# Optimization experiments

Measured on AMD Instinct MI355X. Metric: run time of the kernel, lower is better.

Reference implementation:

```python
import jax, jax.numpy as jnp
import numpy as np

ASPECT = 1.0
SCALE = 0.3
MIN_PATCH_H = 60.0
EPS = 1e-6


def _make_patch_boxes(boxes, H, W):
    # Patcher.create: per detected box, compute [ymin_patch, xmin_patch, patch_h, patch_w]
    ymin, xmin, ymax, xmax = jnp.split(boxes, 4, axis=-1)
    h = ymax - ymin
    w = xmax - xmin
    pw = h * SCALE
    ph = ASPECT * pw
    oy = ymin + h / 2.0
    ox = xmin + w / 2.0
    yp = jnp.maximum(oy - ph / 2.0, 0.0)
    xp = jnp.maximum(ox - pw / 2.0, 0.0)
    yp = jnp.where(yp + ph > H, H - ph, yp)
    xp = jnp.where(xp + pw > W, W - pw, xp)
    return jnp.concatenate([yp, xp, ph, pw], axis=-1)  # [B, N, 4]


def _bilinear(src, rel_y, rel_x, out_h, out_w):
    # tf.image.resize bilinear (half-pixel centers): sample src [P,P,3] at the
    # grid of an (out_h, out_w) resize, evaluated at all H/W image offsets.
    P = src.shape[0]
    sy = jnp.clip((rel_y + 0.5) * P / out_h - 0.5, 0.0, P - 1.0)  # [H]
    sx = jnp.clip((rel_x + 0.5) * P / out_w - 0.5, 0.0, P - 1.0)  # [W]
    y0 = jnp.floor(sy).astype(jnp.int32); y1 = jnp.minimum(y0 + 1, P - 1)
    x0 = jnp.floor(sx).astype(jnp.int32); x1 = jnp.minimum(x0 + 1, P - 1)
    wy = (sy - y0.astype(sy.dtype))[:, None, None]
    wx = (sx - x0.astype(sx.dtype))[None, :, None]
    top = (1.0 - wx) * src[y0[:, None], x0[None, :]] + wx * src[y0[:, None], x1[None, :]]
    bot = (1.0 - wx) * src[y1[:, None], x0[None, :]] + wx * src[y1[:, None], x1[None, :]]
    return (1.0 - wy) * top + wy * bot  # [H, W, 3]


def _forward(images, boxes, patch):
    B, H, W, _ = images.shape
    pboxes = _make_patch_boxes(boxes, float(H), float(W))  # [B, N, 4]
    valid = pboxes[..., 2] > MIN_PATCH_H                    # gather_nd filter
    p_mean = patch.mean((0, 1))
    p_std = patch.std((0, 1)) + EPS
    ys = jnp.arange(H, dtype=jnp.int32)
    xs = jnp.arange(W, dtype=jnp.int32)

    def per_image(image, pbs, vls):
        # serial while_loop over patches: later patches overwrite earlier ones,
        # and histogram match uses the current (already-patched) background.
        def step(img, bv):
            pb, v = bv
            pbi = pb.astype(jnp.int32)  # tf.cast truncation
            y0, x0, ph, pw = pbi[0], pbi[1], pbi[2], pbi[3]
            in_y = (ys >= y0) & (ys < y0 + ph)
            in_x = (xs >= x0) & (xs < x0 + pw)
            mask = in_y[:, None] & in_x[None, :]            # [H, W]
            mf = mask[..., None].astype(img.dtype)
            cnt = jnp.maximum(mask.sum().astype(img.dtype), 1.0)
            bg_mean = (img * mf).sum((0, 1)) / cnt
            bg_std = jnp.sqrt((((img - bg_mean) ** 2) * mf).sum((0, 1)) / cnt) + EPS
            # histogram match (per-channel moment matching) of patch to background
            matched = (patch - p_mean) / p_std * bg_std + bg_mean
            phf = jnp.maximum(ph.astype(img.dtype), 1.0)
            pwf = jnp.maximum(pw.astype(img.dtype), 1.0)
            sampled = _bilinear(matched,
                                (ys - y0).astype(img.dtype),
                                (xs - x0).astype(img.dtype), phf, pwf)
            img = jnp.where(mask[..., None] & v, sampled, img)
            return img, None

        img, _ = jax.lax.scan(step, image, (pbs, vls))
        return img

    return jax.vmap(per_image)(images, pboxes, valid)


def setup_inputs() -> dict:
    key = jax.random.key(0)
    k1, k2, k3 = jax.random.split(key, 3)
    B, N, H, W, P = 16, 16, 512, 512, 512
    images = jax.random.normal(k1, (B, H, W, 3), dtype=jnp.float32)
    u = jax.random.uniform(k2, (B, N, 4), dtype=jnp.float32)
    ymin = u[..., 0] * (H - 320)
    xmin = u[..., 1] * (W - 320)
    h = 150.0 + u[..., 2] * 150.0
    w = 150.0 + u[..., 3] * 150.0
    boxes = jnp.stack([ymin, xmin, ymin + h, xmin + w], axis=-1)
    patch = jax.random.normal(k3, (P, P, 3), dtype=jnp.float32) * 0.5
    return {"images": images, "boxes": boxes, "patch": patch}


def reference(images, boxes, patch):
    return _forward(images, boxes, patch)
```

## Files before the change

kernel.cpp:

```cpp
#include <hip/hip_runtime.h>
#include <math.h>

#define IMG_H 512
#define IMG_W 512
#define PSIZE 512
#define NIMG 16
#define NBOX 16
#define RED_BLOCKS 256
#define ZSPLIT 4

#define WS_PMEAN 0
#define WS_PSTD  3
#define WS_PART  6
#define WS_PAIR  (6 + RED_BLOCKS * 6)
#define WS_COEF  (WS_PAIR + NIMG * NBOX * 17 * ZSPLIT * 8)

struct BoxGeo { int y0, x0, ph, pw, valid; };

__device__ __forceinline__ BoxGeo make_geo(const float* bx) {
    float ymin = bx[0], xmin = bx[1], ymax = bx[2], xmax = bx[3];
    float h = ymax - ymin, w = xmax - xmin;
    float pwf = h * 0.3f;
    float phf = 1.0f * pwf;
    float oy = ymin + h * 0.5f;
    float ox = xmin + w * 0.5f;
    float yp = fmaxf(oy - phf * 0.5f, 0.0f);
    float xp = fmaxf(ox - pwf * 0.5f, 0.0f);
    if (yp + phf > (float)IMG_H) yp = (float)IMG_H - phf;
    if (xp + pwf > (float)IMG_W) xp = (float)IMG_W - pwf;
    BoxGeo g;
    g.y0 = (int)yp; g.x0 = (int)xp;
    g.ph = (int)phf; g.pw = (int)pwf;
    g.valid = (phf > 60.0f) ? 1 : 0;
    return g;
}

__device__ __forceinline__ void bsample(const float* __restrict__ patch,
                                        int relY, int relX, float phf, float pwf,
                                        float s[3]) {
    float sy = ((float)relY + 0.5f) * (float)PSIZE / phf - 0.5f;
    sy = fminf(fmaxf(sy, 0.0f), (float)(PSIZE - 1));
    float sx = ((float)relX + 0.5f) * (float)PSIZE / pwf - 0.5f;
    sx = fminf(fmaxf(sx, 0.0f), (float)(PSIZE - 1));
    int y0 = (int)floorf(sy);
    int y1 = min(y0 + 1, PSIZE - 1);
    int x0 = (int)floorf(sx);
    int x1 = min(x0 + 1, PSIZE - 1);
    float wy = sy - (float)y0;
    float wx = sx - (float)x0;
    const float* p00 = patch + (y0 * PSIZE + x0) * 3;
    const float* p01 = patch + (y0 * PSIZE + x1) * 3;
    const float* p10 = patch + (y1 * PSIZE + x0) * 3;
    const float* p11 = patch + (y1 * PSIZE + x1) * 3;
#pragma unroll
    for (int c = 0; c < 3; ++c) {
        float top = (1.f - wx) * p00[c] + wx * p01[c];
        float bot = (1.f - wx) * p10[c] + wx * p11[c];
        s[c] = (1.f - wy) * top + wy * bot;
    }
}

template<int N, int NWAVES>
__device__ __forceinline__ void block_reduceN(float v[N]) {
    __shared__ float lds[NWAVES][N];
    const int lane = threadIdx.x & 63;
    const int wave = threadIdx.x >> 6;
    __syncthreads();
#pragma unroll
    for (int k = 0; k < N; ++k) {
#pragma unroll
        for (int off = 32; off > 0; off >>= 1)
            v[k] += __shfl_down(v[k], off, 64);
    }
    if (lane == 0) {
#pragma unroll
        for (int k = 0; k < N; ++k) lds[wave][k] = v[k];
    }
    __syncthreads();
    if (wave == 0) {
#pragma unroll
        for (int k = 0; k < N; ++k) {
            float x = (lane < NWAVES) ? lds[lane][k] : 0.0f;
#pragma unroll
            for (int off = 32; off > 0; off >>= 1)
                x += __shfl_down(x, off, 64);
            if (lane == 0) lds[0][k] = x;
        }
    }
    __syncthreads();
#pragma unroll
    for (int k = 0; k < N; ++k) v[k] = lds[0][k];
}

__global__ void patch_stats_partial(const float* __restrict__ patch,
                                    float* __restrict__ ws) {
    const int g = blockIdx.x * 256 + threadIdx.x;
    const float4* p4 = (const float4*)patch;
    float4 a = p4[3 * g], b = p4[3 * g + 1], c = p4[3 * g + 2];
    float v[6];
    v[0] = a.x + a.w + b.z + c.y;
    v[1] = a.y + b.x + b.w + c.z;
    v[2] = a.z + b.y + c.x + c.w;
    v[3] = a.x*a.x + a.w*a.w + b.z*b.z + c.y*c.y;
    v[4] = a.y*a.y + b.x*b.x + b.w*b.w + c.z*c.z;
    v[5] = a.z*a.z + b.y*b.y + c.x*c.x + c.w*c.w;
    block_reduceN<6, 4>(v);
    if (threadIdx.x == 0) {
        float* o = ws + WS_PART + blockIdx.x * 6;
#pragma unroll
        for (int k = 0; k < 6; ++k) o[k] = v[k];
    }
}

__global__ void patch_stats_final(float* __restrict__ ws) {
    float v[6];
    const float* p = ws + WS_PART + threadIdx.x * 6;
#pragma unroll
    for (int k = 0; k < 6; ++k) v[k] = p[k];
    block_reduceN<6, 4>(v);
    if (threadIdx.x == 0) {
        const float n = (float)(PSIZE * PSIZE);
#pragma unroll
        for (int c = 0; c < 3; ++c) {
            float m = v[c] / n;
            float var = v[3 + c] / n - m * m;
            ws[WS_PMEAN + c] = m;
            ws[WS_PSTD + c] = sqrtf(fmaxf(var, 0.f)) + 1e-6f;
        }
    }
}

__launch_bounds__(256)
__global__ void pair_sums(const float* __restrict__ images,
                          const float* __restrict__ boxes,
                          const float* __restrict__ patch,
                          float* __restrict__ ws) {
    const int bi = blockIdx.x;
    const int j_idx = blockIdx.y;
    const int z = blockIdx.z;
    const int b = bi >> 4, i = bi & 15;
    if (j_idx > i) return;

    __shared__ BoxGeo geo[NBOX];
    if (threadIdx.x < NBOX)
        geo[threadIdx.x] = make_geo(boxes + (b * NBOX + threadIdx.x) * 4);
    __syncthreads();

    const BoxGeo gi = geo[i];
    if (!gi.valid) return;

    float* o = ws + WS_PAIR + (((size_t)(b * NBOX + i) * 17 + j_idx) * ZSPLIT + z) * 8;
    const int j = j_idx - 1;

    int ry0 = gi.y0, rx0 = gi.x0;
    int ry1 = gi.y0 + gi.ph, rx1 = gi.x0 + gi.pw;
    int jy0 = 0, jx0 = 0; float jphf = 1.f, jpwf = 1.f;
    if (j >= 0) {
        const BoxGeo gj = geo[j];
        if (!gj.valid) {
            if (threadIdx.x == 0) { for (int k = 0; k < 7; ++k) o[k] = 0.f; }
            return;
        }
        ry0 = max(ry0, gj.y0); rx0 = max(rx0, gj.x0);
        ry1 = min(ry1, gj.y0 + gj.ph); rx1 = min(rx1, gj.x0 + gj.pw);
        jy0 = gj.y0; jx0 = gj.x0;
        jphf = (float)gj.ph; jpwf = (float)gj.pw;
    }
    const int rw = rx1 - rx0, rh = ry1 - ry0;
    if (rw <= 0 || rh <= 0) {
        if (threadIdx.x == 0) { for (int k = 0; k < 7; ++k) o[k] = 0.f; }
        return;
    }
    const int n = rw * rh;
    const float* img = images + (size_t)b * IMG_H * IMG_W * 3;

    float v[7] = {0.f, 0.f, 0.f, 0.f, 0.f, 0.f, 0.f};
    for (int t = z * 256 + threadIdx.x; t < n; t += 256 * ZSPLIT) {
        const int y = ry0 + t / rw;
        const int x = rx0 + t % rw;
        bool inc = true;
        for (int k = j + 1; k < i; ++k) {
            const BoxGeo gk = geo[k];
            if (gk.valid && y >= gk.y0 && y < gk.y0 + gk.ph &&
                x >= gk.x0 && x < gk.x0 + gk.pw) { inc = false; break; }
        }
        if (inc) {
            float s[3];
            if (j >= 0) {
                bsample(patch, y - jy0, x - jx0, jphf, jpwf, s);
            } else {
                const float* p = img + ((size_t)y * IMG_W + x) * 3;
                s[0] = p[0]; s[1] = p[1]; s[2] = p[2];
            }
            v[0] += 1.f;
            v[1] += s[0]; v[2] += s[1]; v[3] += s[2];
            v[4] += s[0]*s[0]; v[5] += s[1]*s[1]; v[6] += s[2]*s[2];
        }
    }
    block_reduceN<7, 4>(v);
    if (threadIdx.x == 0) {
#pragma unroll
        for (int k = 0; k < 7; ++k) o[k] = v[k];
    }
}

__global__ void solve_coeffs(const float* __restrict__ boxes,
                             float* __restrict__ ws) {
    const int b = blockIdx.x;
    const int lane = threadIdx.x;

    BoxGeo g = make_geo(boxes + (b * NBOX + (lane < NBOX ? lane : NBOX - 1)) * 4);
    float pm[3], ps[3];
#pragma unroll
    for (int c = 0; c < 3; ++c) { pm[c] = ws[WS_PMEAN + c]; ps[c] = ws[WS_PSTD + c]; }

    float sc[3] = {0.f, 0.f, 0.f}, of[3] = {0.f, 0.f, 0.f};

    for (int i = 0; i < NBOX; ++i) {
        const int valid_i = __shfl(g.valid, i, 64);
        if (!valid_i) continue;

        float cnt = 0.f, s1[3] = {0.f,0.f,0.f}, s2[3] = {0.f,0.f,0.f};
        if (lane <= i) {
            const float* p = ws + WS_PAIR +
                ((size_t)(b * NBOX + i) * 17 + lane) * ZSPLIT * 8;
#pragma unroll
            for (int zz = 0; zz < ZSPLIT; ++zz) {
                cnt   += p[zz*8 + 0];
                s1[0] += p[zz*8 + 1]; s1[1] += p[zz*8 + 2]; s1[2] += p[zz*8 + 3];
                s2[0] += p[zz*8 + 4]; s2[1] += p[zz*8 + 5]; s2[2] += p[zz*8 + 6];
            }
        }
        float ts[3], tq[3];
#pragma unroll
        for (int c = 0; c < 3; ++c) {
            if (lane == 0) { ts[c] = s1[c]; tq[c] = s2[c]; }
            else {
                ts[c] = sc[c] * s1[c] + of[c] * cnt;
                tq[c] = sc[c]*sc[c]*s2[c] + 2.f*sc[c]*of[c]*s1[c] + of[c]*of[c]*cnt;
            }
        }
#pragma unroll
        for (int c = 0; c < 3; ++c) {
#pragma unroll
            for (int off = 16; off > 0; off >>= 1) {
                ts[c] += __shfl_down(ts[c], off, 32);
                tq[c] += __shfl_down(tq[c], off, 32);
            }
        }
        const int phi = __shfl(g.ph, i, 64);
        const int pwi = __shfl(g.pw, i, 64);
        const float cntf = fmaxf((float)(phi * pwi), 1.0f);
        float nsc[3] = {0.f,0.f,0.f}, nof[3] = {0.f,0.f,0.f};
        if (lane == 0) {
#pragma unroll
            for (int c = 0; c < 3; ++c) {
                float mean = ts[c] / cntf;
                float var = tq[c] / cntf - mean * mean;
                float sd = sqrtf(fmaxf(var, 0.f)) + 1e-6f;
                nsc[c] = sd / ps[c];
                nof[c] = mean - pm[c] * nsc[c];
            }
        }
#pragma unroll
        for (int c = 0; c < 3; ++c) {
            float bs = __shfl(nsc[c], 0, 64);
            float bo = __shfl(nof[c], 0, 64);
            if (lane == i + 1) { sc[c] = bs; of[c] = bo; }
            if (lane == 0) {
                ws[WS_COEF + (size_t)(b * NBOX + i) * 8 + c] = bs;
                ws[WS_COEF + (size_t)(b * NBOX + i) * 8 + 3 + c] = bo;
            }
        }
    }
}

__launch_bounds__(256)
__global__ void render(const float* __restrict__ images,
                       const float* __restrict__ boxes,
                       const float* __restrict__ patch,
                       const float* __restrict__ ws,
                       float* __restrict__ out) {
    const int b = blockIdx.y;
    __shared__ BoxGeo geo[NBOX];
    __shared__ float coef[NBOX][6];
    if (threadIdx.x < NBOX)
        geo[threadIdx.x] = make_geo(boxes + (b * NBOX + threadIdx.x) * 4);
    if (threadIdx.x < NBOX * 6) {
        int i = threadIdx.x / 6, c = threadIdx.x % 6;
        coef[i][c] = ws[WS_COEF + (size_t)(b * NBOX + i) * 8 + c];
    }
    __syncthreads();

    const int q = blockIdx.x * 256 + threadIdx.x;
    const int p0 = q << 2;
    const int y = p0 >> 9, x0 = p0 & 511;

    const float4* src = (const float4*)(images + (size_t)b * IMG_H * IMG_W * 3);
    float4* dst = (float4*)(out + (size_t)b * IMG_H * IMG_W * 3);

    float4 f[3];
    f[0] = src[3*q]; f[1] = src[3*q + 1]; f[2] = src[3*q + 2];
    float* r = (float*)f;

#pragma unroll
    for (int u = 0; u < 4; ++u) {
        const int x = x0 + u;
        int last = -1;
        for (int j = NBOX - 1; j >= 0; --j) {
            const BoxGeo g = geo[j];
            if (g.valid && y >= g.y0 && y < g.y0 + g.ph &&
                x >= g.x0 && x < g.x0 + g.pw) { last = j; break; }
        }
        if (last >= 0) {
            const BoxGeo g = geo[last];
            float s[3];
            bsample(patch, y - g.y0, x - g.x0, (float)g.ph, (float)g.pw, s);
            r[3*u + 0] = s[0] * coef[last][0] + coef[last][3];
            r[3*u + 1] = s[1] * coef[last][1] + coef[last][4];
            r[3*u + 2] = s[2] * coef[last][2] + coef[last][5];
        }
    }
    dst[3*q] = f[0]; dst[3*q + 1] = f[1]; dst[3*q + 2] = f[2];
}

extern "C" void kernel_launch(void* const* d_in, const int* in_sizes, int n_in,
                              void* d_out, int out_size, void* d_ws, size_t ws_size,
                              hipStream_t stream) {
    const float* images = (const float*)d_in[0];
    const float* boxes  = (const float*)d_in[1];
    const float* patch  = (const float*)d_in[2];
    float* out = (float*)d_out;
    float* ws  = (float*)d_ws;

    patch_stats_partial<<<RED_BLOCKS, 256, 0, stream>>>(patch, ws);
    patch_stats_final<<<1, RED_BLOCKS, 0, stream>>>(ws);
    pair_sums<<<dim3(NIMG * NBOX, 17, ZSPLIT), 256, 0, stream>>>(images, boxes, patch, ws);
    solve_coeffs<<<NIMG, 64, 0, stream>>>(boxes, ws);
    render<<<dim3(IMG_H * IMG_W / 4 / 256, NIMG), 256, 0, stream>>>(images, boxes, patch, ws, out);
}
```

Before: 106.0 us.

## Replace full-image render with memcpy plus per-box decal scatter; precompute geometry tasks

```diff
diff --git a/kernel.cpp b/kernel.cpp
--- a/kernel.cpp
+++ b/kernel.cpp
@@ -7,13 +7,17 @@
 #define NIMG 16
 #define NBOX 16
 #define RED_BLOCKS 256
-#define ZSPLIT 4
+#define Z0 8
+#define ZJ 4
+#define SLOTS 72
 
 #define WS_PMEAN 0
 #define WS_PSTD  3
 #define WS_PART  6
-#define WS_PAIR  (6 + RED_BLOCKS * 6)
-#define WS_COEF  (WS_PAIR + NIMG * NBOX * 17 * ZSPLIT * 8)
+#define WS_GEO   1544
+#define WS_TASK  2568
+#define WS_PAIR  37384
+#define WS_COEF  (WS_PAIR + 256 * SLOTS * 8)
 
 struct BoxGeo { int y0, x0, ph, pw, valid; };
 
@@ -92,6 +96,46 @@
     for (int k = 0; k < N; ++k) v[k] = lds[0][k];
 }
 
+__global__ void setup_geo(const float* __restrict__ boxes,
+                          float* __restrict__ ws) {
+    int* iws = (int*)ws;
+    const int tid = threadIdx.x;
+    if (tid < NIMG * NBOX) {
+        BoxGeo g = make_geo(boxes + tid * 4);
+        ((int4*)(iws + WS_GEO))[tid] =
+            make_int4(g.y0, g.x0, g.valid ? g.ph : -1, g.pw);
+    }
+    for (int t = tid; t < NIMG * NBOX * 17; t += 256) {
+        const int bi = t / 17, j_idx = t % 17;
+        const int b = bi >> 4, i = bi & 15;
+        int d[8] = {0, 0, 0, 0, 0, 0, -1, 0};
+        if (j_idx <= i) {
+            BoxGeo gi = make_geo(boxes + (b * NBOX + i) * 4);
+            if (gi.valid) {
+                int ry0 = gi.y0, rx0 = gi.x0;
+                int ry1 = gi.y0 + gi.ph, rx1 = gi.x0 + gi.pw;
+                bool ok = true;
+                if (j_idx >= 1) {
+                    BoxGeo gj = make_geo(boxes + (b * NBOX + j_idx - 1) * 4);
+                    if (!gj.valid) ok = false;
+                    else {
+                        ry0 = max(ry0, gj.y0); rx0 = max(rx0, gj.x0);
+                        ry1 = min(ry1, gj.y0 + gj.ph);
+                        rx1 = min(rx1, gj.x0 + gj.pw);
+                        d[4] = gj.y0; d[5] = gj.x0; d[6] = gj.ph; d[7] = gj.pw;
+                    }
+                }
+                if (ok && ry1 > ry0 && rx1 > rx0) {
+                    d[0] = ry0; d[1] = rx0; d[2] = rx1 - rx0; d[3] = ry1 - ry0;
+                }
+            }
+        }
+        int* o = iws + WS_TASK + t * 8;
+#pragma unroll
+        for (int k = 0; k < 8; ++k) o[k] = d[k];
+    }
+}
+
 __global__ void patch_stats_partial(const float* __restrict__ patch,
                                     float* __restrict__ ws) {
     const int g = blockIdx.x * 256 + threadIdx.x;
@@ -132,61 +176,43 @@
 
 __launch_bounds__(256)
 __global__ void pair_sums(const float* __restrict__ images,
-                          const float* __restrict__ boxes,
                           const float* __restrict__ patch,
                           float* __restrict__ ws) {
-    const int bi = blockIdx.x;
-    const int j_idx = blockIdx.y;
-    const int z = blockIdx.z;
-    const int b = bi >> 4, i = bi & 15;
+    const int bi = blockIdx.x, j_idx = blockIdx.y, z = blockIdx.z;
+    const int i = bi & 15;
     if (j_idx > i) return;
-
-    __shared__ BoxGeo geo[NBOX];
+    if (j_idx >= 1 && z >= ZJ) return;
+    const int* iws = (const int*)ws;
+    const int* d = iws + WS_TASK + (bi * 17 + j_idx) * 8;
+    const int rw = d[2];
+    if (rw <= 0) return;
+    const int ry0 = d[0], rx0 = d[1], rh = d[3];
+    const int jy0 = d[4], jx0 = d[5], jph = d[6], jpw = d[7];
+
+    __shared__ int4 sgeo[NBOX];
     if (threadIdx.x < NBOX)
-        geo[threadIdx.x] = make_geo(boxes + (b * NBOX + threadIdx.x) * 4);
-    __syncthreads();
-
-    const BoxGeo gi = geo[i];
-    if (!gi.valid) return;
-
-    float* o = ws + WS_PAIR + (((size_t)(b * NBOX + i) * 17 + j_idx) * ZSPLIT + z) * 8;
-    const int j = j_idx - 1;
-
-    int ry0 = gi.y0, rx0 = gi.x0;
-    int ry1 = gi.y0 + gi.ph, rx1 = gi.x0 + gi.pw;
-    int jy0 = 0, jx0 = 0; float jphf = 1.f, jpwf = 1.f;
-    if (j >= 0) {
-        const BoxGeo gj = geo[j];
-        if (!gj.valid) {
-            if (threadIdx.x == 0) { for (int k = 0; k < 7; ++k) o[k] = 0.f; }
-            return;
-        }
-        ry0 = max(ry0, gj.y0); rx0 = max(rx0, gj.x0);
-        ry1 = min(ry1, gj.y0 + gj.ph); rx1 = min(rx1, gj.x0 + gj.pw);
-        jy0 = gj.y0; jx0 = gj.x0;
-        jphf = (float)gj.ph; jpwf = (float)gj.pw;
-    }
-    const int rw = rx1 - rx0, rh = ry1 - ry0;
-    if (rw <= 0 || rh <= 0) {
-        if (threadIdx.x == 0) { for (int k = 0; k < 7; ++k) o[k] = 0.f; }
-        return;
-    }
+        sgeo[threadIdx.x] =
+            ((const int4*)(iws + WS_GEO))[(bi >> 4) * NBOX + threadIdx.x];
+    __syncthreads();
+
     const int n = rw * rh;
-    const float* img = images + (size_t)b * IMG_H * IMG_W * 3;
+    const float* img = images + (size_t)(bi >> 4) * IMG_H * IMG_W * 3;
+    const float jphf = (float)jph, jpwf = (float)jpw;
+    const int nz = (j_idx == 0) ? Z0 : ZJ;
 
     float v[7] = {0.f, 0.f, 0.f, 0.f, 0.f, 0.f, 0.f};
-    for (int t = z * 256 + threadIdx.x; t < n; t += 256 * ZSPLIT) {
+    for (int t = z * 256 + threadIdx.x; t < n; t += 256 * nz) {
         const int y = ry0 + t / rw;
         const int x = rx0 + t % rw;
         bool inc = true;
-        for (int k = j + 1; k < i; ++k) {
-            const BoxGeo gk = geo[k];
-            if (gk.valid && y >= gk.y0 && y < gk.y0 + gk.ph &&
-                x >= gk.x0 && x < gk.x0 + gk.pw) { inc = false; break; }
+        for (int k = j_idx; k < i; ++k) {
+            const int4 g = sgeo[k];
+            if (g.z > 0 && y >= g.x && y < g.x + g.z &&
+                x >= g.y && x < g.y + g.w) { inc = false; break; }
         }
         if (inc) {
             float s[3];
-            if (j >= 0) {
+            if (jph > 0) {
                 bsample(patch, y - jy0, x - jx0, jphf, jpwf, s);
             } else {
                 const float* p = img + ((size_t)y * IMG_W + x) * 3;
@@ -199,6 +225,8 @@
     }
     block_reduceN<7, 4>(v);
     if (threadIdx.x == 0) {
+        const int slot = (j_idx == 0) ? z : (Z0 + (j_idx - 1) * ZJ + z);
+        float* o = ws + WS_PAIR + ((size_t)bi * SLOTS + slot) * 8;
 #pragma unroll
         for (int k = 0; k < 7; ++k) o[k] = v[k];
     }
@@ -222,10 +250,11 @@
 
         float cnt = 0.f, s1[3] = {0.f,0.f,0.f}, s2[3] = {0.f,0.f,0.f};
         if (lane <= i) {
+            const int slot0 = (lane == 0) ? 0 : (Z0 + (lane - 1) * ZJ);
+            const int nz = (lane == 0) ? Z0 : ZJ;
             const float* p = ws + WS_PAIR +
-                ((size_t)(b * NBOX + i) * 17 + lane) * ZSPLIT * 8;
-#pragma unroll
-            for (int zz = 0; zz < ZSPLIT; ++zz) {
+                ((size_t)(b * NBOX + i) * SLOTS + slot0) * 8;
+            for (int zz = 0; zz < nz; ++zz) {
                 cnt   += p[zz*8 + 0];
                 s1[0] += p[zz*8 + 1]; s1[1] += p[zz*8 + 2]; s1[2] += p[zz*8 + 3];
                 s2[0] += p[zz*8 + 4]; s2[1] += p[zz*8 + 5]; s2[2] += p[zz*8 + 6];
@@ -276,52 +305,44 @@
 }
 
 __launch_bounds__(256)
-__global__ void render(const float* __restrict__ images,
-                       const float* __restrict__ boxes,
-                       const float* __restrict__ patch,
-                       const float* __restrict__ ws,
-                       float* __restrict__ out) {
-    const int b = blockIdx.y;
-    __shared__ BoxGeo geo[NBOX];
-    __shared__ float coef[NBOX][6];
+__global__ void decal(const float* __restrict__ patch,
+                      const float* __restrict__ ws,
+                      float* __restrict__ out) {
+    const int bi = blockIdx.x;
+    const int b = bi >> 4, i = bi & 15;
+    const int* iws = (const int*)ws;
+    __shared__ int4 sgeo[NBOX];
+    __shared__ float scoef[6];
     if (threadIdx.x < NBOX)
-        geo[threadIdx.x] = make_geo(boxes + (b * NBOX + threadIdx.x) * 4);
-    if (threadIdx.x < NBOX * 6) {
-        int i = threadIdx.x / 6, c = threadIdx.x % 6;
-        coef[i][c] = ws[WS_COEF + (size_t)(b * NBOX + i) * 8 + c];
-    }
-    __syncthreads();
-
-    const int q = blockIdx.x * 256 + threadIdx.x;
-    const int p0 = q << 2;
-    const int y = p0 >> 9, x0 = p0 & 511;
-
-    const float4* src = (const float4*)(images + (size_t)b * IMG_H * IMG_W * 3);
-    float4* dst = (float4*)(out + (size_t)b * IMG_H * IMG_W * 3);
-
-    float4 f[3];
-    f[0] = src[3*q]; f[1] = src[3*q + 1]; f[2] = src[3*q + 2];
-    float* r = (float*)f;
-
-#pragma unroll
-    for (int u = 0; u < 4; ++u) {
-        const int x = x0 + u;
-        int last = -1;
-        for (int j = NBOX - 1; j >= 0; --j) {
-            const BoxGeo g = geo[j];
-            if (g.valid && y >= g.y0 && y < g.y0 + g.ph &&
-                x >= g.x0 && x < g.x0 + g.pw) { last = j; break; }
-        }
-        if (last >= 0) {
-            const BoxGeo g = geo[last];
+        sgeo[threadIdx.x] = ((const int4*)(iws + WS_GEO))[b * NBOX + threadIdx.x];
+    if (threadIdx.x >= 32 && threadIdx.x < 38)
+        scoef[threadIdx.x - 32] = ws[WS_COEF + (size_t)bi * 8 + (threadIdx.x - 32)];
+    __syncthreads();
+    const int4 gi = sgeo[i];
+    if (gi.z <= 0) return;
+    const int y0 = gi.x, x0 = gi.y, ph = gi.z, pw = gi.w;
+    const int n = ph * pw;
+    const float phf = (float)ph, pwf = (float)pw;
+    float* img = out + (size_t)b * IMG_H * IMG_W * 3;
+
+    for (int t = blockIdx.y * 256 + threadIdx.x; t < n; t += 256 * 8) {
+        const int y = y0 + t / pw;
+        const int x = x0 + t % pw;
+        bool cov = false;
+        for (int k = i + 1; k < NBOX; ++k) {
+            const int4 g = sgeo[k];
+            if (g.z > 0 && y >= g.x && y < g.x + g.z &&
+                x >= g.y && x < g.y + g.w) { cov = true; break; }
+        }
+        if (!cov) {
             float s[3];
-            bsample(patch, y - g.y0, x - g.x0, (float)g.ph, (float)g.pw, s);
-            r[3*u + 0] = s[0] * coef[last][0] + coef[last][3];
-            r[3*u + 1] = s[1] * coef[last][1] + coef[last][4];
-            r[3*u + 2] = s[2] * coef[last][2] + coef[last][5];
-        }
-    }
-    dst[3*q] = f[0]; dst[3*q + 1] = f[1]; dst[3*q + 2] = f[2];
+            bsample(patch, y - y0, x - x0, phf, pwf, s);
+            float* o = img + ((size_t)y * IMG_W + x) * 3;
+            o[0] = s[0] * scoef[0] + scoef[3];
+            o[1] = s[1] * scoef[1] + scoef[4];
+            o[2] = s[2] * scoef[2] + scoef[5];
+        }
+    }
 }
 
 extern "C" void kernel_launch(void* const* d_in, const int* in_sizes, int n_in,
@@ -333,9 +354,13 @@
     float* out = (float*)d_out;
     float* ws  = (float*)d_ws;
 
+    hipMemsetAsync(ws + WS_PAIR, 0, (size_t)256 * SLOTS * 8 * sizeof(float), stream);
+    setup_geo<<<1, 256, 0, stream>>>(boxes, ws);
     patch_stats_partial<<<RED_BLOCKS, 256, 0, stream>>>(patch, ws);
     patch_stats_final<<<1, RED_BLOCKS, 0, stream>>>(ws);
-    pair_sums<<<dim3(NIMG * NBOX, 17, ZSPLIT), 256, 0, stream>>>(images, boxes, patch, ws);
+    hipMemcpyAsync(out, images, (size_t)NIMG * IMG_H * IMG_W * 3 * sizeof(float),
+                   hipMemcpyDeviceToDevice, stream);
+    pair_sums<<<dim3(NIMG * NBOX, 17, Z0), 256, 0, stream>>>(images, patch, ws);
     solve_coeffs<<<NIMG, 64, 0, stream>>>(boxes, ws);
-    render<<<dim3(IMG_H * IMG_W / 4 / 256, NIMG), 256, 0, stream>>>(images, boxes, patch, ws, out);
-}
+    decal<<<dim3(NIMG * NBOX, 8), 256, 0, stream>>>(patch, ws, out);
+}
```

Result: slower. 134.7 us (+27.1%).
